# Kernel optimization log

Measured on AMD Instinct MI355X. Metric: run time of the kernel, lower is better.

The kernel has to match this reference:

```python
import jax, jax.numpy as jnp
import numpy as np
from jax import lax

B, T, D, H = 4, 4096, 1024, 8
DK, DV = 1024, 2048          # expand_k=1.0, expand_v=2.0
RANK, MAXL, LOOPD = 16, 8, 128  # lora_rank, max_loops, dim*loop_dim_fraction
THRESH = 0.99
EPS = 1e-6
GK_SCALE = 16.0              # GLA forget-gate temperature


def setup_inputs() -> dict:
    key = jax.random.key(0)
    ks = jax.random.split(key, 16)
    r = lambda i, shape, s=0.02: jax.random.normal(ks[i], shape, jnp.float32) * s
    return {
        "h": jax.random.normal(ks[0], (B, T, D), jnp.float32),
        "e": jax.random.normal(ks[1], (B, T, D), jnp.float32),
        "norm_w": jnp.ones((D,), jnp.float32),
        "out_norm_w": jnp.ones((D,), jnp.float32),
        "Wq": r(2, (D, DK)), "Wk": r(3, (D, DK)), "Wv": r(4, (D, DV)),
        "Wgk": r(5, (D, DK)), "Wg": r(6, (D, DV)), "Wo": r(7, (DV, D)),
        "lora_A": r(8, (MAXL, D, RANK)), "lora_B": r(9, (MAXL, RANK, D)),
        "inj_A": 0.9 * jnp.eye(D, dtype=jnp.float32) + r(10, (D, D)),
        "inj_B": r(11, (D, D)),
        "act_w": r(12, (D,)),
        "act_b": jnp.full((), -2.0, jnp.float32),  # gradual halting
        "loop_table": r(13, (MAXL, LOOPD)),
        "n_loops": 4,
    }


def rmsnorm(x, w):
    return x * lax.rsqrt(jnp.mean(x * x, axis=-1, keepdims=True) + EPS) * w


def gla(x, Wq, Wk, Wv, Wgk, Wg, Wo, num_heads):
    """Gated Linear Attention: data-dependent forget gates, linear-time recurrent scan."""
    b, t, d = x.shape
    dk, dv = Wq.shape[1], Wv.shape[1]
    dkh, dvh = dk // num_heads, dv // num_heads
    q = (x @ Wq).reshape(b, t, num_heads, dkh) * (dkh ** -0.5)
    k = (x @ Wk).reshape(b, t, num_heads, dkh)
    v = (x @ Wv).reshape(b, t, num_heads, dvh)
    # forget gate alpha in (0,1): exp(logsigmoid(gk)/16)
    alpha = jnp.exp(jax.nn.log_sigmoid(x @ Wgk) / GK_SCALE).reshape(b, t, num_heads, dkh)

    def step(S, qkva):  # S: (b, H, dkh, dvh)
        qt, kt, vt, at = qkva
        S = at[..., None] * S + kt[..., None] * vt[..., None, :]
        ot = jnp.einsum('bhk,bhkv->bhv', qt, S)
        return S, ot

    S0 = jnp.zeros((b, num_heads, dkh, dvh), x.dtype)
    xs = (jnp.swapaxes(q, 0, 1), jnp.swapaxes(k, 0, 1),
          jnp.swapaxes(v, 0, 1), jnp.swapaxes(alpha, 0, 1))
    _, o = lax.scan(step, S0, xs)                  # o: (t, b, H, dvh)
    o = jnp.swapaxes(o, 0, 1).reshape(b, t, dv)
    o = o * jax.nn.silu(x @ Wg)                    # output gate
    return o @ Wo


def reference(h, e, norm_w, out_norm_w, Wq, Wk, Wv, Wgk, Wg, Wo,
              lora_A, lora_B, inj_A, inj_B, act_w, act_b, loop_table, n_loops):
    b, t_len, d = h.shape
    halted = jnp.zeros((b, t_len), bool)
    cum = jnp.zeros((b, t_len), h.dtype)
    h_out = jnp.zeros_like(h)
    loopd = loop_table.shape[1]
    for t in range(n_loops):  # small fixed depth loop (structurally distinct LoRA/embed per t)
        # loop index embedding on first loopd channels
        h = h.at[..., :loopd].add(loop_table[t])
        h_norm = rmsnorm(h + e, norm_w)
        g = gla(h_norm, Wq, Wk, Wv, Wgk, Wg, Wo, H)   # dropout: eval mode (identity)
        g = g + (g @ lora_A[t]) @ lora_B[t]            # depth LoRA
        h = h @ inj_A.T + e @ inj_B.T + g              # LTI injection: A.h + B.e + gla
        # ACT halting accumulate
        p = jax.nn.sigmoid(h @ act_w + act_b)          # (b, t_len)
        running = ~halted
        p_eff = jnp.where(running, p, jnp.zeros_like(p))
        new_cum = cum + p_eff
        newly = running & (new_cum >= THRESH)
        w = jnp.where(newly, 1.0 - cum, p_eff)         # remainder for newly-halted
        h_out = h_out + w[..., None] * h
        cum = new_cum
        halted = halted | newly
    return rmsnorm(h_out, out_norm_w)
```

## Files before the change

kernel.cpp:

```cpp
#include <hip/hip_runtime.h>

#define BB 4
#define TT 4096
#define DD 1024
#define HH 8
#define DKK 1024
#define DVV 2048
#define MR (BB*TT)
#define DKH 128
#define DVH 256
#define NLOOPS 4
#define LCH 128
#define NCH (TT/LCH)
#define PADW 136
#define NPROJ 7168

#define WS_NEED 662310912ull

__device__ __attribute__((aligned(256))) unsigned char g_ws[WS_NEED];

typedef __bf16 bf16x8 __attribute__((ext_vector_type(8)));
typedef float  f32x4  __attribute__((ext_vector_type(4)));

__device__ __forceinline__ unsigned short f2bfu(float f) {
    unsigned int u = __builtin_bit_cast(unsigned int, f);
    u += 0x7fffu + ((u >> 16) & 1u);
    return (unsigned short)(u >> 16);
}
__device__ __forceinline__ float bfu2f(unsigned short s) {
    unsigned int u = ((unsigned int)s) << 16;
    return __builtin_bit_cast(float, u);
}

__device__ __forceinline__ void gld_lds16(const void* g, void* l) {
    __builtin_amdgcn_global_load_lds(
        (__attribute__((address_space(1))) void*)const_cast<void*>(g),
        (__attribute__((address_space(3))) void*)l, 16, 0, 0);
}

__global__ __launch_bounds__(256) void k_transpose_bf16(
    const float* __restrict__ in, unsigned short* __restrict__ out, int K, int N)
{
    __shared__ float tile[64][65];
    int k0 = blockIdx.y * 64, n0 = blockIdx.x * 64;
    int tx = threadIdx.x & 63, ty = threadIdx.x >> 6;
    #pragma unroll
    for (int r = 0; r < 64; r += 4)
        tile[ty + r][tx] = in[(size_t)(k0 + ty + r) * N + n0 + tx];
    __syncthreads();
    #pragma unroll
    for (int r = 0; r < 64; r += 4)
        out[(size_t)(n0 + ty + r) * K + k0 + tx] = f2bfu(tile[tx][ty + r]);
}

__global__ __launch_bounds__(256) void k_conv_e(
    const float* __restrict__ e, unsigned short* __restrict__ he)
{
    size_t gid = (size_t)blockIdx.x * 256 + threadIdx.x;
    size_t b4 = gid * 4;
    size_t row = b4 >> 10; int col = (int)(b4 & 1023);
    float4 v = *(const float4*)&e[row * 1024 + col];
    *(ushort4*)&he[row * 2048 + 1024 + col] =
        make_ushort4(f2bfu(v.x), f2bfu(v.y), f2bfu(v.z), f2bfu(v.w));
}

__global__ __launch_bounds__(256) void k_conv_injcomb(
    const float* __restrict__ injA, const float* __restrict__ injB,
    unsigned short* __restrict__ WinjT, float* __restrict__ diag)
{
    int idx = blockIdx.x * 256 + threadIdx.x;
    int i = idx >> 10, j = idx & 1023;
    float va = injA[idx], vb = injB[idx];
    unsigned short ua;
    if (i == j) { diag[i] = va; ua = 0; }
    else        { ua = f2bfu(va); }
    WinjT[(size_t)i * 2048 + j] = ua;
    WinjT[(size_t)i * 2048 + 1024 + j] = f2bfu(vb);
}

__global__ __launch_bounds__(256) void k_prep(
    float* __restrict__ h, const float* __restrict__ e,
    const float* __restrict__ norm_w, const float* __restrict__ ltab,
    unsigned short* __restrict__ he, unsigned short* __restrict__ xn_bf)
{
    int row = blockIdx.x, tid = threadIdx.x;
    size_t base = (size_t)row * DD + tid * 4;
    float4 hv = *(float4*)&h[base];
    if (tid < 32) {
        float4 lv = *(const float4*)&ltab[tid * 4];
        hv.x += lv.x; hv.y += lv.y; hv.z += lv.z; hv.w += lv.w;
        *(float4*)&h[base] = hv;
    }
    float4 ev = *(const float4*)&e[base];
    float sx = hv.x + ev.x, sy = hv.y + ev.y, sz = hv.z + ev.z, sw = hv.w + ev.w;
    float partial = sx*sx + sy*sy + sz*sz + sw*sw;
    __shared__ float red[256];
    red[tid] = partial; __syncthreads();
    for (int st = 128; st > 0; st >>= 1) {
        if (tid < st) red[tid] += red[tid + st];
        __syncthreads();
    }
    float rms = rsqrtf(red[0] * (1.0f / DD) + 1e-6f);
    float4 wv = *(const float4*)&norm_w[tid * 4];
    *(ushort4*)&xn_bf[base] = make_ushort4(
        f2bfu(sx * rms * wv.x), f2bfu(sy * rms * wv.y),
        f2bfu(sz * rms * wv.z), f2bfu(sw * rms * wv.w));
    *(ushort4*)&he[(size_t)row * 2048 + tid * 4] =
        make_ushort4(f2bfu(hv.x), f2bfu(hv.y), f2bfu(hv.z), f2bfu(hv.w));
}

template<int KB>
__device__ __forceinline__ void gemm8_core(
    const char* __restrict__ Ab, const char* __restrict__ Bb,
    int bm, int bn, char* sm, f32x4 (&acc)[8][4])
{
    constexpr int NKT = KB / 128;
    const int tid = threadIdx.x;
    const int lane = tid & 63;
    const int wave = tid >> 6;
    const int wm = wave >> 2, wn = wave & 3;
    const int ln15 = lane & 15, q4 = lane >> 4;
    const int xorv = (ln15 & 7) << 4;
    const int xc0 = (q4 * 16) ^ xorv;
    const int xc1 = (64 + q4 * 16) ^ xorv;

    const int L0 = tid * 16;
    const int L1 = 8192 + tid * 16;
    const int lin0 = L0 ^ (((L0 >> 7) & 7) << 4);
    const int lin1 = L1 ^ (((L1 >> 7) & 7) << 4);
    const int sr0 = lin0 >> 7, sc0 = lin0 & 127;
    const int sr1 = lin1 >> 7, sc1 = lin1 & 127;

    bf16x8 av[4][2];
    bf16x8 bv[2][2][2];

    auto STAGE = [&](const char* gb, int row0, int kcol, int region) {
        gld_lds16(gb + (size_t)(row0 + sr0) * KB + (kcol + sc0), sm + region + L0);
        gld_lds16(gb + (size_t)(row0 + sr1) * KB + (kcol + sc1), sm + region + L1);
    };

#define LD_AV(CB, MH) \
    _Pragma("unroll") \
    for (int i2 = 0; i2 < 4; ++i2) { \
        const char* rp = sm + (CB) + ((MH) * 16384) \
                       + ((wm * 64 + i2 * 16 + ln15) * 128); \
        av[i2][0] = *(const bf16x8*)(rp + xc0); \
        av[i2][1] = *(const bf16x8*)(rp + xc1); \
    }
#define LD_BV(CB, NH) \
    _Pragma("unroll") \
    for (int j2 = 0; j2 < 2; ++j2) { \
        const char* rp = sm + (CB) + 32768 + ((NH) * 16384) \
                       + ((wn * 32 + j2 * 16 + ln15) * 128); \
        bv[NH][j2][0] = *(const bf16x8*)(rp + xc0); \
        bv[NH][j2][1] = *(const bf16x8*)(rp + xc1); \
    }
#define MFMA_Q(MH, NH) \
    __builtin_amdgcn_s_setprio(1); \
    _Pragma("unroll") \
    for (int i2 = 0; i2 < 4; ++i2) \
        _Pragma("unroll") \
        for (int j2 = 0; j2 < 2; ++j2) { \
            acc[(MH)*4+i2][(NH)*2+j2] = __builtin_amdgcn_mfma_f32_16x16x32_bf16( \
                av[i2][0], bv[NH][j2][0], acc[(MH)*4+i2][(NH)*2+j2], 0, 0, 0); \
            acc[(MH)*4+i2][(NH)*2+j2] = __builtin_amdgcn_mfma_f32_16x16x32_bf16( \
                av[i2][1], bv[NH][j2][1], acc[(MH)*4+i2][(NH)*2+j2], 0, 0, 0); \
        } \
    __builtin_amdgcn_s_setprio(0);

    STAGE(Ab, bm,       0, 0);
    STAGE(Bb, bn,       0, 32768);
    STAGE(Bb, bn + 128, 0, 49152);
    STAGE(Ab, bm + 128, 0, 16384);

    #pragma unroll 2
    for (int kt = 0; kt < NKT - 1; ++kt) {
        const int cb = (kt & 1) << 16;
        const int sb = cb ^ 65536;
        const int kcol = (kt + 1) * 128;
        STAGE(Ab, bm, kcol, sb);
        asm volatile("s_waitcnt vmcnt(6)" ::: "memory");
        __builtin_amdgcn_s_barrier();
        LD_AV(cb, 0)
        LD_BV(cb, 0)
        MFMA_Q(0, 0)
        STAGE(Bb, bn, kcol, sb + 32768);
        asm volatile("s_waitcnt vmcnt(6)" ::: "memory");
        __builtin_amdgcn_s_barrier();
        LD_BV(cb, 1)
        MFMA_Q(0, 1)
        STAGE(Bb, bn + 128, kcol, sb + 49152);
        asm volatile("s_waitcnt vmcnt(6)" ::: "memory");
        __builtin_amdgcn_s_barrier();
        LD_AV(cb, 1)
        MFMA_Q(1, 1)
        STAGE(Ab, bm + 128, kcol, sb + 16384);
        MFMA_Q(1, 0)
    }
    {
        const int cb = ((NKT - 1) & 1) << 16;
        asm volatile("s_waitcnt vmcnt(4)" ::: "memory");
        __builtin_amdgcn_s_barrier();
        LD_AV(cb, 0)
        LD_BV(cb, 0)
        MFMA_Q(0, 0)
        asm volatile("s_waitcnt vmcnt(2)" ::: "memory");
        __builtin_amdgcn_s_barrier();
        LD_BV(cb, 1)
        MFMA_Q(0, 1)
        asm volatile("s_waitcnt vmcnt(0)" ::: "memory");
        __builtin_amdgcn_s_barrier();
        LD_AV(cb, 1)
        MFMA_Q(1, 1)
        MFMA_Q(1, 0)
    }
#undef LD_AV
#undef LD_BV
#undef MFMA_Q
}

__global__ __launch_bounds__(512, 2) void k_gemm_proj8(
    const unsigned short* __restrict__ A, const unsigned short* __restrict__ Bt,
    unsigned short* __restrict__ qout, unsigned short* __restrict__ kout,
    float* __restrict__ lgout, unsigned short* __restrict__ vout,
    unsigned short* __restrict__ xgout, float qscale)
{
    extern __shared__ char sm[];
    int bid = blockIdx.x;
    int nb = (bid & 7) * 224 + (bid >> 3);
    int bm = (nb / 28) * 256, bn = (nb % 28) * 256;

    f32x4 acc[8][4];
    #pragma unroll
    for (int i = 0; i < 8; ++i)
        #pragma unroll
        for (int j = 0; j < 4; ++j) { f32x4 z = {0,0,0,0}; acc[i][j] = z; }

    gemm8_core<2048>((const char*)A, (const char*)Bt, bm, bn, sm, acc);

    const int tid = threadIdx.x, lane = tid & 63, wave = tid >> 6;
    const int wm = wave >> 2, wn = wave & 3;
    const int ln15 = lane & 15, q4 = lane >> 4;

    if (bn >= 2048 && bn < 3072) {
        int cb = bn - 2048;
        #pragma unroll
        for (int fm = 0; fm < 8; ++fm) {
            int mh = fm >> 2, i2 = fm & 3;
            int rowb = bm + mh * 128 + wm * 64 + i2 * 16 + q4 * 4;
            #pragma unroll
            for (int fn = 0; fn < 4; ++fn) {
                int nh = fn >> 1, j2 = fn & 1;
                int col = cb + nh * 128 + wn * 32 + j2 * 16 + ln15;
                #pragma unroll
                for (int r = 0; r < 4; ++r) {
                    float v = acc[fm][fn][r];
                    v = (fminf(v, 0.f) - log1pf(expf(-fabsf(v)))) * 0.0625f;
                    lgout[(size_t)(rowb + r) * 1024 + col] = v;
                }
            }
        }
    } else {
        unsigned short* obuf; int stride, cb;
        float scale = 1.f;
        if (bn < 1024)      { obuf = qout;  stride = 1024; cb = bn;        scale = qscale; }
        else if (bn < 2048) { obuf = kout;  stride = 1024; cb = bn - 1024; }
        else if (bn < 5120) { obuf = vout;  stride = 2048; cb = bn - 3072; }
        else                { obuf = xgout; stride = 2048; cb = bn - 5120; }
        #pragma unroll
        for (int fm = 0; fm < 8; ++fm) {
            int mh = fm >> 2, i2 = fm & 3;
            int rowb = bm + mh * 128 + wm * 64 + i2 * 16 + q4 * 4;
            #pragma unroll
            for (int fn = 0; fn < 4; ++fn) {
                int nh = fn >> 1, j2 = fn & 1;
                int col = cb + nh * 128 + wn * 32 + j2 * 16 + ln15;
                #pragma unroll
                for (int r = 0; r < 4; ++r)
                    obuf[(size_t)(rowb + r) * stride + col] =
                        f2bfu(acc[fm][fn][r] * scale);
            }
        }
    }
}

template<int HASADD, int HASDIAG, int KB>
__global__ __launch_bounds__(512, 2) void k_gemm8_f32(
    const unsigned short* __restrict__ A, const unsigned short* __restrict__ Bt,
    float* __restrict__ out, const float* __restrict__ addend,
    const float* __restrict__ hsrc, const float* __restrict__ diag, int N)
{
    extern __shared__ char sm[];
    int bid = blockIdx.x;
    int cpx = gridDim.x >> 3;
    int nb = (bid & 7) * cpx + (bid >> 3);
    int nbn = N >> 8;
    int bm = (nb / nbn) * 256, bn = (nb % nbn) * 256;

    f32x4 acc[8][4];
    #pragma unroll
    for (int i = 0; i < 8; ++i)
        #pragma unroll
        for (int j = 0; j < 4; ++j) { f32x4 z = {0,0,0,0}; acc[i][j] = z; }

    gemm8_core<KB>((const char*)A, (const char*)Bt, bm, bn, sm, acc);

    const int tid = threadIdx.x, lane = tid & 63, wave = tid >> 6;
    const int wm = wave >> 2, wn = wave & 3;
    const int ln15 = lane & 15, q4 = lane >> 4;

    #pragma unroll
    for (int fm = 0; fm < 8; ++fm) {
        int mh = fm >> 2, i2 = fm & 3;
        int rowb = bm + mh * 128 + wm * 64 + i2 * 16 + q4 * 4;
        #pragma unroll
        for (int fn = 0; fn < 4; ++fn) {
            int nh = fn >> 1, j2 = fn & 1;
            int col = bn + nh * 128 + wn * 32 + j2 * 16 + ln15;
            float dg = 0.f;
            if (HASDIAG) dg = diag[col];
            #pragma unroll
            for (int r = 0; r < 4; ++r) {
                size_t oi = (size_t)(rowb + r) * N + col;
                float v = acc[fm][fn][r];
                if (HASDIAG) v += hsrc[oi] * dg;
                if (HASADD)  v += addend[oi];
                out[oi] = v;
            }
        }
    }
}

__global__ __launch_bounds__(256) void k_c1(
    const float* __restrict__ lg, unsigned short* __restrict__ q,
    unsigned short* __restrict__ kk, float* __restrict__ dLe)
{
    int chunk = blockIdx.x;
    int bh = blockIdx.y * 2 + (threadIdx.x >> 7);
    int b = bh >> 3, h = bh & 7;
    int i = threadIdx.x & 127;
    size_t r0 = (size_t)b * TT + (size_t)chunk * LCH;
    float c = 0.f, e = 1.f;
    for (int t = 0; t < LCH; ++t) {
        size_t off = (r0 + t) * DKK + h * DKH + i;
        c += lg[off];
        e = __expf(c);
        float ei = __expf(-c);
        q[off] = f2bfu(bfu2f(q[off]) * e);
        kk[off] = f2bfu(bfu2f(kk[off]) * ei);
    }
    dLe[((size_t)chunk * 32 + bh) * DKH + i] = e;
}

__global__ __launch_bounds__(256, 1) void k_c2(
    const unsigned short* __restrict__ q, const unsigned short* __restrict__ kk,
    const unsigned short* __restrict__ v, unsigned short* __restrict__ ob,
    float* __restrict__ U)
{
    extern __shared__ unsigned short smd[];
    unsigned short* lQ  = smd;
    unsigned short* lK  = smd + LCH * PADW;
    unsigned short* lKT = smd + 2 * LCH * PADW;
    unsigned short* lVT = smd + 3 * LCH * PADW;

    int chunk = blockIdx.x, bh = blockIdx.y;
    int b = bh >> 3, h = bh & 7;
    int tid = threadIdx.x, lane = tid & 63, wave = tid >> 6;
    int wm = wave >> 1, wn = wave & 1;
    int quad = lane >> 4, mr = lane & 15;
    size_t r0 = (size_t)b * TT + (size_t)chunk * LCH;

    #pragma unroll
    for (int ps = 0; ps < 8; ++ps) {
        int idx = ps * 256 + tid;
        int row = idx >> 4, c8 = (idx & 15) * 8;
        size_t g = (r0 + row) * DKK + h * DKH + c8;
        *(int4*)&lQ[row * PADW + c8] = *(const int4*)&q[g];
        union { int4 w; unsigned short u[8]; } tmp;
        tmp.w = *(const int4*)&kk[g];
        *(int4*)&lK[row * PADW + c8] = tmp.w;
        #pragma unroll
        for (int u2 = 0; u2 < 8; ++u2)
            lKT[(c8 + u2) * PADW + row] = tmp.u[u2];
    }
    __syncthreads();

    f32x4 pa[4][4];
    #pragma unroll
    for (int i = 0; i < 4; ++i)
        #pragma unroll
        for (int j = 0; j < 4; ++j) { f32x4 z = {0,0,0,0}; pa[i][j] = z; }
    for (int k0 = 0; k0 < DKH; k0 += 32) {
        bf16x8 av[4], bv[4];
        #pragma unroll
        for (int t2 = 0; t2 < 4; ++t2) {
            av[t2] = *(const bf16x8*)&lQ[(wm * 64 + t2 * 16 + mr) * PADW + k0 + quad * 8];
            bv[t2] = *(const bf16x8*)&lK[(wn * 64 + t2 * 16 + mr) * PADW + k0 + quad * 8];
        }
        #pragma unroll
        for (int tm = 0; tm < 4; ++tm)
            #pragma unroll
            for (int tn = 0; tn < 4; ++tn)
                pa[tm][tn] = __builtin_amdgcn_mfma_f32_16x16x32_bf16(
                    av[tm], bv[tn], pa[tm][tn], 0, 0, 0);
    }
    __syncthreads();

    #pragma unroll
    for (int tm = 0; tm < 4; ++tm)
        #pragma unroll
        for (int tn = 0; tn < 4; ++tn)
            #pragma unroll
            for (int r = 0; r < 4; ++r) {
                int trow = wm * 64 + tm * 16 + quad * 4 + r;
                int scol = wn * 64 + tn * 16 + mr;
                float pv = (trow >= scol) ? pa[tm][tn][r] : 0.f;
                lQ[trow * PADW + scol] = f2bfu(pv);
            }
    #pragma unroll
    for (int ps = 0; ps < 8; ++ps) {
        int idx = ps * 256 + tid;
        int s = idx >> 4, j8 = (idx & 15) * 8;
        size_t g = (r0 + s) * DVV + h * DVH + j8;
        union { int4 w; unsigned short u[8]; } tmp;
        tmp.w = *(const int4*)&v[g];
        #pragma unroll
        for (int u2 = 0; u2 < 8; ++u2)
            lVT[(j8 + u2) * PADW + s] = tmp.u[u2];
    }
    __syncthreads();

    #pragma unroll 1
    for (int panel = 0; panel < 2; ++panel) {
        f32x4 oa[4][4], ua[4][4];
        #pragma unroll
        for (int i = 0; i < 4; ++i)
            #pragma unroll
            for (int j = 0; j < 4; ++j) { f32x4 z = {0,0,0,0}; oa[i][j] = z; ua[i][j] = z; }
        for (int k0 = 0; k0 < LCH; k0 += 32) {
            bf16x8 pv[4], kt[4], vb[4];
            #pragma unroll
            for (int t2 = 0; t2 < 4; ++t2) {
                pv[t2] = *(const bf16x8*)&lQ [(wm * 64 + t2 * 16 + mr) * PADW + k0 + quad * 8];
                kt[t2] = *(const bf16x8*)&lKT[(wm * 64 + t2 * 16 + mr) * PADW + k0 + quad * 8];
                vb[t2] = *(const bf16x8*)&lVT[(wn * 64 + t2 * 16 + mr) * PADW + k0 + quad * 8];
            }
            #pragma unroll
            for (int tm = 0; tm < 4; ++tm)
                #pragma unroll
                for (int tn = 0; tn < 4; ++tn) {
                    oa[tm][tn] = __builtin_amdgcn_mfma_f32_16x16x32_bf16(
                        pv[tm], vb[tn], oa[tm][tn], 0, 0, 0);
                    ua[tm][tn] = __builtin_amdgcn_mfma_f32_16x16x32_bf16(
                        kt[tm], vb[tn], ua[tm][tn], 0, 0, 0);
                }
        }
        #pragma unroll
        for (int tm = 0; tm < 4; ++tm)
            #pragma unroll
            for (int tn = 0; tn < 4; ++tn)
                #pragma unroll
                for (int r = 0; r < 4; ++r) {
                    int m_ = wm * 64 + tm * 16 + quad * 4 + r;
                    int j_ = panel * 128 + wn * 64 + tn * 16 + mr;
                    ob[(r0 + m_) * DVV + h * DVH + j_] = f2bfu(oa[tm][tn][r]);
                    U[(((size_t)chunk * 32 + bh) * DKH + m_) * DVH + j_] = ua[tm][tn][r];
                }
        __syncthreads();
        if (panel == 0) {
            #pragma unroll
            for (int ps = 0; ps < 8; ++ps) {
                int idx = ps * 256 + tid;
                int s = idx >> 4, j8 = (idx & 15) * 8;
                size_t g = (r0 + s) * DVV + h * DVH + 128 + j8;
                union { int4 w; unsigned short u[8]; } tmp;
                tmp.w = *(const int4*)&v[g];
                #pragma unroll
                for (int u2 = 0; u2 < 8; ++u2)
                    lVT[(j8 + u2) * PADW + s] = tmp.u[u2];
            }
            __syncthreads();
        }
    }
}

__global__ __launch_bounds__(256) void k_c3(
    float* __restrict__ U, const float* __restrict__ dLe)
{
    int gid = blockIdx.x * 256 + threadIdx.x;
    int bh = gid >> 13;
    int rem = gid & 8191;
    int i = rem >> 6, j4 = rem & 63;
    float4 S = make_float4(0.f, 0.f, 0.f, 0.f);
    for (int c = 0; c < NCH; ++c) {
        size_t off = (((size_t)c * 32 + bh) * DKH + i) * DVH + j4 * 4;
        float4 u = *(float4*)&U[off];
        *(float4*)&U[off] = S;
        float d = dLe[((size_t)c * 32 + bh) * DKH + i];
        S.x = d * (S.x + u.x); S.y = d * (S.y + u.y);
        S.z = d * (S.z + u.z); S.w = d * (S.w + u.w);
    }
}

__global__ __launch_bounds__(256, 1) void k_c4(
    const unsigned short* __restrict__ q, const float* __restrict__ S,
    unsigned short* __restrict__ ob, const unsigned short* __restrict__ xg)
{
    extern __shared__ unsigned short smd[];
    unsigned short* lQ  = smd;
    unsigned short* lST = smd + LCH * PADW;

    int chunk = blockIdx.x, bh = blockIdx.y;
    int b = bh >> 3, h = bh & 7;
    int tid = threadIdx.x, lane = tid & 63, wave = tid >> 6;
    int wm = wave >> 1, wn = wave & 1;
    int quad = lane >> 4, mr = lane & 15;
    size_t r0 = (size_t)b * TT + (size_t)chunk * LCH;

    #pragma unroll
    for (int ps = 0; ps < 8; ++ps) {
        int idx = ps * 256 + tid;
        int row = idx >> 4, c8 = (idx & 15) * 8;
        size_t g = (r0 + row) * DKK + h * DKH + c8;
        *(int4*)&lQ[row * PADW + c8] = *(const int4*)&q[g];
    }

    #pragma unroll 1
    for (int panel = 0; panel < 2; ++panel) {
        __syncthreads();
        #pragma unroll
        for (int ps = 0; ps < 16; ++ps) {
            int idx = ps * 256 + tid;
            int i = idx >> 5, j4 = idx & 31;
            float4 sv = *(const float4*)&S[(((size_t)chunk * 32 + bh) * DKH + i) * DVH
                                           + panel * 128 + j4 * 4];
            lST[(j4 * 4 + 0) * PADW + i] = f2bfu(sv.x);
            lST[(j4 * 4 + 1) * PADW + i] = f2bfu(sv.y);
            lST[(j4 * 4 + 2) * PADW + i] = f2bfu(sv.z);
            lST[(j4 * 4 + 3) * PADW + i] = f2bfu(sv.w);
        }
        __syncthreads();

        f32x4 oa[4][4];
        #pragma unroll
        for (int i = 0; i < 4; ++i)
            #pragma unroll
            for (int j = 0; j < 4; ++j) { f32x4 z = {0,0,0,0}; oa[i][j] = z; }
        for (int k0 = 0; k0 < DKH; k0 += 32) {
            bf16x8 av[4], bv[4];
            #pragma unroll
            for (int t2 = 0; t2 < 4; ++t2) {
                av[t2] = *(const bf16x8*)&lQ [(wm * 64 + t2 * 16 + mr) * PADW + k0 + quad * 8];
                bv[t2] = *(const bf16x8*)&lST[(wn * 64 + t2 * 16 + mr) * PADW + k0 + quad * 8];
            }
            #pragma unroll
            for (int tm = 0; tm < 4; ++tm)
                #pragma unroll
                for (int tn = 0; tn < 4; ++tn)
                    oa[tm][tn] = __builtin_amdgcn_mfma_f32_16x16x32_bf16(
                        av[tm], bv[tn], oa[tm][tn], 0, 0, 0);
        }
        #pragma unroll
        for (int tm = 0; tm < 4; ++tm)
            #pragma unroll
            for (int tn = 0; tn < 4; ++tn)
                #pragma unroll
                for (int r = 0; r < 4; ++r) {
                    int t_ = wm * 64 + tm * 16 + quad * 4 + r;
                    int j_ = panel * 128 + wn * 64 + tn * 16 + mr;
                    size_t oi = (r0 + t_) * DVV + h * DVH + j_;
                    float ov = bfu2f(ob[oi]) + oa[tm][tn][r];
                    float xf = bfu2f(xg[oi]);
                    ob[oi] = f2bfu(ov * xf / (1.f + expf(-xf)));
                }
    }
}

__global__ __launch_bounds__(256) void k_lora1(
    const float* __restrict__ G, const float* __restrict__ A, float* __restrict__ tmp)
{
    int row = blockIdx.x * 4 + (threadIdx.x >> 6);
    int lane = threadIdx.x & 63;
    float acc[16];
    #pragma unroll
    for (int r = 0; r < 16; ++r) acc[r] = 0.f;
    const float* grow = G + (size_t)row * DD;
    for (int k2 = lane; k2 < DD; k2 += 64) {
        float g = grow[k2];
        const float4* ar = (const float4*)(A + k2 * 16);
        float4 a0 = ar[0], a1 = ar[1], a2 = ar[2], a3 = ar[3];
        acc[0] = fmaf(g, a0.x, acc[0]);  acc[1] = fmaf(g, a0.y, acc[1]);
        acc[2] = fmaf(g, a0.z, acc[2]);  acc[3] = fmaf(g, a0.w, acc[3]);
        acc[4] = fmaf(g, a1.x, acc[4]);  acc[5] = fmaf(g, a1.y, acc[5]);
        acc[6] = fmaf(g, a1.z, acc[6]);  acc[7] = fmaf(g, a1.w, acc[7]);
        acc[8] = fmaf(g, a2.x, acc[8]);  acc[9] = fmaf(g, a2.y, acc[9]);
        acc[10] = fmaf(g, a2.z, acc[10]); acc[11] = fmaf(g, a2.w, acc[11]);
        acc[12] = fmaf(g, a3.x, acc[12]); acc[13] = fmaf(g, a3.y, acc[13]);
        acc[14] = fmaf(g, a3.z, acc[14]); acc[15] = fmaf(g, a3.w, acc[15]);
    }
    #pragma unroll
    for (int off = 32; off >= 1; off >>= 1)
        #pragma unroll
        for (int r = 0; r < 16; ++r) acc[r] += __shfl_xor(acc[r], off);
    if (lane == 0) {
        #pragma unroll
        for (int r = 0; r < 16; ++r) tmp[(size_t)row * 16 + r] = acc[r];
    }
}

__global__ __launch_bounds__(256) void k_lora2(
    float* __restrict__ G, const float* __restrict__ tmp, const float* __restrict__ Bm)
{
    int row = blockIdx.x, tid = threadIdx.x;
    __shared__ float t16[16];
    if (tid < 16) t16[tid] = tmp[(size_t)row * 16 + tid];
    __syncthreads();
    size_t base = (size_t)row * DD + tid * 4;
    float4 acc = *(float4*)&G[base];
    #pragma unroll
    for (int r = 0; r < 16; ++r) {
        float tv = t16[r];
        float4 bv = *(const float4*)&Bm[r * DD + tid * 4];
        acc.x = fmaf(tv, bv.x, acc.x); acc.y = fmaf(tv, bv.y, acc.y);
        acc.z = fmaf(tv, bv.z, acc.z); acc.w = fmaf(tv, bv.w, acc.w);
    }
    *(float4*)&G[base] = acc;
}

__global__ __launch_bounds__(256) void k_act(
    const float* __restrict__ h, const float* __restrict__ act_w,
    const float* __restrict__ act_b, float* __restrict__ out,
    float* __restrict__ cum, int* __restrict__ halted)
{
    int row = blockIdx.x, tid = threadIdx.x;
    size_t base = (size_t)row * DD + tid * 4;
    float4 hv = *(const float4*)&h[base];
    float4 wv = *(const float4*)&act_w[tid * 4];
    float partial = hv.x*wv.x + hv.y*wv.y + hv.z*wv.z + hv.w*wv.w;
    __shared__ float red[256];
    __shared__ float s_cm;
    __shared__ int s_hl;
    if (tid == 0) { s_cm = cum[row]; s_hl = halted[row]; }
    red[tid] = partial; __syncthreads();
    for (int st = 128; st > 0; st >>= 1) {
        if (tid < st) red[tid] += red[tid + st];
        __syncthreads();
    }
    float p = 1.f / (1.f + expf(-(red[0] + act_b[0])));
    float cm = s_cm;
    int hl = s_hl;
    float p_eff = hl ? 0.f : p;
    float ncum = cm + p_eff;
    int newly = (!hl) && (ncum >= 0.99f);
    float w = newly ? (1.f - cm) : p_eff;
    float4 ho = *(float4*)&out[base];
    ho.x += w * hv.x; ho.y += w * hv.y; ho.z += w * hv.z; ho.w += w * hv.w;
    *(float4*)&out[base] = ho;
    if (tid == 0) { cum[row] = ncum; halted[row] = hl | newly; }
}

__global__ __launch_bounds__(256) void k_final(
    float* __restrict__ io, const float* __restrict__ w)
{
    int row = blockIdx.x, tid = threadIdx.x;
    size_t base = (size_t)row * DD + tid * 4;
    float4 hv = *(const float4*)&io[base];
    float partial = hv.x*hv.x + hv.y*hv.y + hv.z*hv.z + hv.w*hv.w;
    __shared__ float red[256];
    red[tid] = partial; __syncthreads();
    for (int st = 128; st > 0; st >>= 1) {
        if (tid < st) red[tid] += red[tid + st];
        __syncthreads();
    }
    float rms = rsqrtf(red[0] * (1.0f / DD) + 1e-6f);
    float4 wv = *(const float4*)&w[tid * 4];
    float4 o = make_float4(hv.x*rms*wv.x, hv.y*rms*wv.y, hv.z*rms*wv.z, hv.w*rms*wv.w);
    *(float4*)&io[base] = o;
}

extern "C" void kernel_launch(void* const* d_in, const int* in_sizes, int n_in,
                              void* d_out, int out_size, void* d_ws, size_t ws_size,
                              hipStream_t stream)
{
    const float* in_h       = (const float*)d_in[0];
    const float* in_e       = (const float*)d_in[1];
    const float* norm_w     = (const float*)d_in[2];
    const float* out_norm_w = (const float*)d_in[3];
    const float* Wq   = (const float*)d_in[4];
    const float* Wk   = (const float*)d_in[5];
    const float* Wv   = (const float*)d_in[6];
    const float* Wgk  = (const float*)d_in[7];
    const float* Wg   = (const float*)d_in[8];
    const float* Wo   = (const float*)d_in[9];
    const float* lora_A = (const float*)d_in[10];
    const float* lora_B = (const float*)d_in[11];
    const float* inj_A  = (const float*)d_in[12];
    const float* inj_B  = (const float*)d_in[13];
    const float* act_w  = (const float*)d_in[14];
    const float* act_b  = (const float*)d_in[15];
    const float* loop_table = (const float*)d_in[16];

    char* p;
    if (ws_size >= WS_NEED) {
        p = (char*)d_ws;
    } else {
        void* sym = nullptr;
        hipGetSymbolAddress(&sym, HIP_SYMBOL(g_ws));
        p = (char*)sym;
    }

    float* h      = (float*)p;            p += (size_t)MR * DD * 4;
    unsigned short* he_bf = (unsigned short*)p; p += (size_t)MR * 2048 * 2;
    unsigned short* xn_bf = (unsigned short*)p; p += (size_t)MR * DD * 2;
    unsigned short* q_bf  = (unsigned short*)p; p += (size_t)MR * DKK * 2;
    unsigned short* k_bf  = (unsigned short*)p; p += (size_t)MR * DKK * 2;
    unsigned short* v_bf  = (unsigned short*)p; p += (size_t)MR * DVV * 2;
    unsigned short* xg_bf = (unsigned short*)p; p += (size_t)MR * DVV * 2;
    float* lgbuf  = (float*)p;            p += (size_t)MR * DKK * 4;
    unsigned short* ob0   = (unsigned short*)p; p += (size_t)MR * DVV * 2;
    float* U      = (float*)p;            p += (size_t)NCH * 32 * DKH * DVH * 4;
    float* dLe    = (float*)p;            p += (size_t)NCH * 32 * DKH * 4;
    unsigned short* WprojT = (unsigned short*)p; p += (size_t)NPROJ * DKK * 2;
    unsigned short* WoT    = (unsigned short*)p; p += (size_t)DD * DVV * 2;
    unsigned short* WinjT  = (unsigned short*)p; p += (size_t)DD * 2048 * 2;
    float* diagA = (float*)p;             p += DD * 4;
    float* tmp16 = (float*)p;             p += (size_t)MR * 16 * 4;
    float* cum   = (float*)p;             p += MR * 4;
    int*   halted = (int*)p;              p += MR * 4;
    float* g2 = lgbuf;
    float* h_out = (float*)d_out;

    hipMemcpyAsync(h, in_h, (size_t)MR * DD * 4, hipMemcpyDeviceToDevice, stream);
    hipMemsetAsync(h_out, 0, (size_t)MR * DD * 4, stream);
    hipMemsetAsync(cum, 0, MR * 4, stream);
    hipMemsetAsync(halted, 0, MR * 4, stream);

    k_transpose_bf16<<<dim3(16, 16), 256, 0, stream>>>(Wq,  WprojT,              DD, DKK);
    k_transpose_bf16<<<dim3(16, 16), 256, 0, stream>>>(Wk,  WprojT + 1024*1024,  DD, DKK);
    k_transpose_bf16<<<dim3(16, 16), 256, 0, stream>>>(Wgk, WprojT + 2048*1024,  DD, DKK);
    k_transpose_bf16<<<dim3(32, 16), 256, 0, stream>>>(Wv,  WprojT + 3072*1024,  DD, DVV);
    k_transpose_bf16<<<dim3(32, 16), 256, 0, stream>>>(Wg,  WprojT + (size_t)5120*1024, DD, DVV);
    k_transpose_bf16<<<dim3(16, 32), 256, 0, stream>>>(Wo,  WoT, DVV, DD);
    k_conv_injcomb<<<4096, 256, 0, stream>>>(inj_A, inj_B, WinjT, diagA);
    k_conv_e<<<MR * DD / 1024, 256, 0, stream>>>(in_e, he_bf);

    const float qscale = 0.08838834764831845f;

    for (int t = 0; t < NLOOPS; ++t) {
        k_prep<<<MR, 256, 0, stream>>>(h, in_e, norm_w, loop_table + t * 128, he_bf, xn_bf);

        k_gemm_proj8<<<1792, 512, 131072, stream>>>(
            xn_bf, WprojT, q_bf, k_bf, lgbuf, v_bf, xg_bf, qscale);

        k_c1<<<dim3(NCH, 16), 256, 0, stream>>>(lgbuf, q_bf, k_bf, dLe);
        k_c2<<<dim3(NCH, 32), 256, 4 * LCH * PADW * 2, stream>>>(
            q_bf, k_bf, v_bf, ob0, U);
        k_c3<<<1024, 256, 0, stream>>>(U, dLe);
        k_c4<<<dim3(NCH, 32), 256, 2 * LCH * PADW * 2, stream>>>(q_bf, U, ob0, xg_bf);

        k_gemm8_f32<0, 0, 4096><<<256, 512, 131072, stream>>>(
            ob0, WoT, g2, nullptr, nullptr, nullptr, DD);

        k_lora1<<<MR / 4, 256, 0, stream>>>(g2, lora_A + (size_t)t * DD * 16, tmp16);
        k_lora2<<<MR, 256, 0, stream>>>(g2, tmp16, lora_B + (size_t)t * 16 * DD);

        k_gemm8_f32<1, 1, 4096><<<256, 512, 131072, stream>>>(
            he_bf, WinjT, h, g2, h, diagA, DD);

        k_act<<<MR, 256, 0, stream>>>(h, act_w, act_b, h_out, cum, halted);
    }

    k_final<<<MR, 256, 0, stream>>>(h_out, out_norm_w);
}
```

Measured before the change: 4.177 ms.

## Interleave GEMM epilogue with final MFMA quadrants and widen chunk kernel to 8 waves

The shared GEMM core now takes an epilogue callback that stores each accumulator quadrant as soon as its last MFMAs finish. This lets global stores overlap with the remaining matrix math instead of running after it. The first-quadrant B load is hoisted, which removes one barrier/waitcnt per k-step, and the wait counts are retuned to match. The intra-chunk kernel k_c2 moves from 4 to 8 waves per block, with each wave covering half the columns, to raise parallelism. The risks are more register pressure, and a stale-LDS hazard if the new wait counts do not cover the hoisted B loads.

```diff
diff --git a/kernel.cpp b/kernel.cpp
--- a/kernel.cpp
+++ b/kernel.cpp
@@ -22,6 +22,8 @@
 typedef __bf16 bf16x8 __attribute__((ext_vector_type(8)));
 typedef float  f32x4  __attribute__((ext_vector_type(4)));
 
+template<int N> struct IC { static constexpr int v = N; };
+
 __device__ __forceinline__ unsigned short f2bfu(float f) {
     unsigned int u = __builtin_bit_cast(unsigned int, f);
     u += 0x7fffu + ((u >> 16) & 1u);
@@ -108,36 +110,6 @@
     *(ushort4*)&he[(size_t)row * 2048 + tid * 4] =
         make_ushort4(f2bfu(hv.x), f2bfu(hv.y), f2bfu(hv.z), f2bfu(hv.w));
 }
-
-template<int KB>
-__device__ __forceinline__ void gemm8_core(
-    const char* __restrict__ Ab, const char* __restrict__ Bb,
-    int bm, int bn, char* sm, f32x4 (&acc)[8][4])
-{
-    constexpr int NKT = KB / 128;
-    const int tid = threadIdx.x;
-    const int lane = tid & 63;
-    const int wave = tid >> 6;
-    const int wm = wave >> 2, wn = wave & 3;
-    const int ln15 = lane & 15, q4 = lane >> 4;
-    const int xorv = (ln15 & 7) << 4;
-    const int xc0 = (q4 * 16) ^ xorv;
-    const int xc1 = (64 + q4 * 16) ^ xorv;
-
-    const int L0 = tid * 16;
-    const int L1 = 8192 + tid * 16;
-    const int lin0 = L0 ^ (((L0 >> 7) & 7) << 4);
-    const int lin1 = L1 ^ (((L1 >> 7) & 7) << 4);
-    const int sr0 = lin0 >> 7, sc0 = lin0 & 127;
-    const int sr1 = lin1 >> 7, sc1 = lin1 & 127;
-
-    bf16x8 av[4][2];
-    bf16x8 bv[2][2][2];
-
-    auto STAGE = [&](const char* gb, int row0, int kcol, int region) {
-        gld_lds16(gb + (size_t)(row0 + sr0) * KB + (kcol + sc0), sm + region + L0);
-        gld_lds16(gb + (size_t)(row0 + sr1) * KB + (kcol + sc1), sm + region + L1);
-    };
 
 #define LD_AV(CB, MH) \
     _Pragma("unroll") \
@@ -168,6 +140,37 @@
         } \
     __builtin_amdgcn_s_setprio(0);
 
+template<int KB, class EPI>
+__device__ __forceinline__ void gemm8_core(
+    const char* __restrict__ Ab, const char* __restrict__ Bb,
+    int bm, int bn, char* sm, f32x4 (&acc)[8][4], EPI&& epi)
+{
+    constexpr int NKT = KB / 128;
+    const int tid = threadIdx.x;
+    const int lane = tid & 63;
+    const int wave = tid >> 6;
+    const int wm = wave >> 2, wn = wave & 3;
+    const int ln15 = lane & 15, q4 = lane >> 4;
+    (void)q4;
+    const int xorv = (ln15 & 7) << 4;
+    const int xc0 = (q4 * 16) ^ xorv;
+    const int xc1 = (64 + q4 * 16) ^ xorv;
+
+    const int L0 = tid * 16;
+    const int L1 = 8192 + tid * 16;
+    const int lin0 = L0 ^ (((L0 >> 7) & 7) << 4);
+    const int lin1 = L1 ^ (((L1 >> 7) & 7) << 4);
+    const int sr0 = lin0 >> 7, sc0 = lin0 & 127;
+    const int sr1 = lin1 >> 7, sc1 = lin1 & 127;
+
+    bf16x8 av[4][2];
+    bf16x8 bv[2][2][2];
+
+    auto STAGE = [&](const char* gb, int row0, int kcol, int region) {
+        gld_lds16(gb + (size_t)(row0 + sr0) * KB + (kcol + sc0), sm + region + L0);
+        gld_lds16(gb + (size_t)(row0 + sr1) * KB + (kcol + sc1), sm + region + L1);
+    };
+
     STAGE(Ab, bm,       0, 0);
     STAGE(Bb, bn,       0, 32768);
     STAGE(Bb, bn + 128, 0, 49152);
@@ -179,15 +182,13 @@
         const int sb = cb ^ 65536;
         const int kcol = (kt + 1) * 128;
         STAGE(Ab, bm, kcol, sb);
-        asm volatile("s_waitcnt vmcnt(6)" ::: "memory");
+        asm volatile("s_waitcnt vmcnt(4)" ::: "memory");
         __builtin_amdgcn_s_barrier();
         LD_AV(cb, 0)
         LD_BV(cb, 0)
+        LD_BV(cb, 1)
         MFMA_Q(0, 0)
         STAGE(Bb, bn, kcol, sb + 32768);
-        asm volatile("s_waitcnt vmcnt(6)" ::: "memory");
-        __builtin_amdgcn_s_barrier();
-        LD_BV(cb, 1)
         MFMA_Q(0, 1)
         STAGE(Bb, bn + 128, kcol, sb + 49152);
         asm volatile("s_waitcnt vmcnt(6)" ::: "memory");
@@ -199,24 +200,23 @@
     }
     {
         const int cb = ((NKT - 1) & 1) << 16;
-        asm volatile("s_waitcnt vmcnt(4)" ::: "memory");
+        asm volatile("s_waitcnt vmcnt(2)" ::: "memory");
         __builtin_amdgcn_s_barrier();
         LD_AV(cb, 0)
         LD_BV(cb, 0)
+        LD_BV(cb, 1)
         MFMA_Q(0, 0)
-        asm volatile("s_waitcnt vmcnt(2)" ::: "memory");
-        __builtin_amdgcn_s_barrier();
-        LD_BV(cb, 1)
+        epi(IC<0>{}, IC<0>{});
         MFMA_Q(0, 1)
+        epi(IC<0>{}, IC<1>{});
         asm volatile("s_waitcnt vmcnt(0)" ::: "memory");
         __builtin_amdgcn_s_barrier();
         LD_AV(cb, 1)
         MFMA_Q(1, 1)
+        epi(IC<1>{}, IC<1>{});
         MFMA_Q(1, 0)
-    }
-#undef LD_AV
-#undef LD_BV
-#undef MFMA_Q
+        epi(IC<1>{}, IC<0>{});
+    }
 }
 
 __global__ __launch_bounds__(512, 2) void k_gemm_proj8(
@@ -230,58 +230,60 @@
     int nb = (bid & 7) * 224 + (bid >> 3);
     int bm = (nb / 28) * 256, bn = (nb % 28) * 256;
 
-    f32x4 acc[8][4];
-    #pragma unroll
-    for (int i = 0; i < 8; ++i)
-        #pragma unroll
-        for (int j = 0; j < 4; ++j) { f32x4 z = {0,0,0,0}; acc[i][j] = z; }
-
-    gemm8_core<2048>((const char*)A, (const char*)Bt, bm, bn, sm, acc);
-
     const int tid = threadIdx.x, lane = tid & 63, wave = tid >> 6;
     const int wm = wave >> 2, wn = wave & 3;
     const int ln15 = lane & 15, q4 = lane >> 4;
 
-    if (bn >= 2048 && bn < 3072) {
-        int cb = bn - 2048;
-        #pragma unroll
-        for (int fm = 0; fm < 8; ++fm) {
-            int mh = fm >> 2, i2 = fm & 3;
-            int rowb = bm + mh * 128 + wm * 64 + i2 * 16 + q4 * 4;
-            #pragma unroll
-            for (int fn = 0; fn < 4; ++fn) {
-                int nh = fn >> 1, j2 = fn & 1;
-                int col = cb + nh * 128 + wn * 32 + j2 * 16 + ln15;
+    const bool islg = (bn >= 2048 && bn < 3072);
+    const int lgc = bn - 2048;
+    unsigned short* obuf = qout; int stride = 1024, cbc = bn;
+    float scale = 1.f;
+    if (bn < 1024)          { scale = qscale; }
+    else if (bn < 2048)     { obuf = kout;  cbc = bn - 1024; }
+    else if (bn >= 5120)    { obuf = xgout; stride = 2048; cbc = bn - 5120; }
+    else if (bn >= 3072)    { obuf = vout;  stride = 2048; cbc = bn - 3072; }
+
+    f32x4 acc[8][4];
+    #pragma unroll
+    for (int i = 0; i < 8; ++i)
+        #pragma unroll
+        for (int j = 0; j < 4; ++j) { f32x4 z = {0,0,0,0}; acc[i][j] = z; }
+
+    auto epi = [&](auto MHt, auto NHt) {
+        constexpr int mh = decltype(MHt)::v;
+        constexpr int nh = decltype(NHt)::v;
+        if (islg) {
+            #pragma unroll
+            for (int i2 = 0; i2 < 4; ++i2) {
+                int rowb = bm + mh * 128 + wm * 64 + i2 * 16 + q4 * 4;
                 #pragma unroll
-                for (int r = 0; r < 4; ++r) {
-                    float v = acc[fm][fn][r];
-                    v = (fminf(v, 0.f) - log1pf(expf(-fabsf(v)))) * 0.0625f;
-                    lgout[(size_t)(rowb + r) * 1024 + col] = v;
+                for (int j2 = 0; j2 < 2; ++j2) {
+                    int col = lgc + nh * 128 + wn * 32 + j2 * 16 + ln15;
+                    #pragma unroll
+                    for (int r = 0; r < 4; ++r) {
+                        float v = acc[mh * 4 + i2][nh * 2 + j2][r];
+                        v = (fminf(v, 0.f) - log1pf(expf(-fabsf(v)))) * 0.0625f;
+                        lgout[(size_t)(rowb + r) * 1024 + col] = v;
+                    }
+                }
+            }
+        } else {
+            #pragma unroll
+            for (int i2 = 0; i2 < 4; ++i2) {
+                int rowb = bm + mh * 128 + wm * 64 + i2 * 16 + q4 * 4;
+                #pragma unroll
+                for (int j2 = 0; j2 < 2; ++j2) {
+                    int col = cbc + nh * 128 + wn * 32 + j2 * 16 + ln15;
+                    #pragma unroll
+                    for (int r = 0; r < 4; ++r)
+                        obuf[(size_t)(rowb + r) * stride + col] =
+                            f2bfu(acc[mh * 4 + i2][nh * 2 + j2][r] * scale);
                 }
             }
         }
-    } else {
-        unsigned short* obuf; int stride, cb;
-        float scale = 1.f;
-        if (bn < 1024)      { obuf = qout;  stride = 1024; cb = bn;        scale = qscale; }
-        else if (bn < 2048) { obuf = kout;  stride = 1024; cb = bn - 1024; }
-        else if (bn < 5120) { obuf = vout;  stride = 2048; cb = bn - 3072; }
-        else                { obuf = xgout; stride = 2048; cb = bn - 5120; }
-        #pragma unroll
-        for (int fm = 0; fm < 8; ++fm) {
-            int mh = fm >> 2, i2 = fm & 3;
-            int rowb = bm + mh * 128 + wm * 64 + i2 * 16 + q4 * 4;
-            #pragma unroll
-            for (int fn = 0; fn < 4; ++fn) {
-                int nh = fn >> 1, j2 = fn & 1;
-                int col = cb + nh * 128 + wn * 32 + j2 * 16 + ln15;
-                #pragma unroll
-                for (int r = 0; r < 4; ++r)
-                    obuf[(size_t)(rowb + r) * stride + col] =
-                        f2bfu(acc[fm][fn][r] * scale);
-            }
-        }
-    }
+    };
+
+    gemm8_core<2048>((const char*)A, (const char*)Bt, bm, bn, sm, acc, epi);
 }
 
 template<int HASADD, int HASDIAG, int KB>
@@ -297,39 +299,45 @@
     int nbn = N >> 8;
     int bm = (nb / nbn) * 256, bn = (nb % nbn) * 256;
 
-    f32x4 acc[8][4];
-    #pragma unroll
-    for (int i = 0; i < 8; ++i)
-        #pragma unroll
-        for (int j = 0; j < 4; ++j) { f32x4 z = {0,0,0,0}; acc[i][j] = z; }
-
-    gemm8_core<KB>((const char*)A, (const char*)Bt, bm, bn, sm, acc);
-
     const int tid = threadIdx.x, lane = tid & 63, wave = tid >> 6;
     const int wm = wave >> 2, wn = wave & 3;
     const int ln15 = lane & 15, q4 = lane >> 4;
 
-    #pragma unroll
-    for (int fm = 0; fm < 8; ++fm) {
-        int mh = fm >> 2, i2 = fm & 3;
-        int rowb = bm + mh * 128 + wm * 64 + i2 * 16 + q4 * 4;
-        #pragma unroll
-        for (int fn = 0; fn < 4; ++fn) {
-            int nh = fn >> 1, j2 = fn & 1;
-            int col = bn + nh * 128 + wn * 32 + j2 * 16 + ln15;
-            float dg = 0.f;
-            if (HASDIAG) dg = diag[col];
-            #pragma unroll
-            for (int r = 0; r < 4; ++r) {
-                size_t oi = (size_t)(rowb + r) * N + col;
-                float v = acc[fm][fn][r];
-                if (HASDIAG) v += hsrc[oi] * dg;
-                if (HASADD)  v += addend[oi];
-                out[oi] = v;
+    f32x4 acc[8][4];
+    #pragma unroll
+    for (int i = 0; i < 8; ++i)
+        #pragma unroll
+        for (int j = 0; j < 4; ++j) { f32x4 z = {0,0,0,0}; acc[i][j] = z; }
+
+    auto epi = [&](auto MHt, auto NHt) {
+        constexpr int mh = decltype(MHt)::v;
+        constexpr int nh = decltype(NHt)::v;
+        #pragma unroll
+        for (int i2 = 0; i2 < 4; ++i2) {
+            int rowb = bm + mh * 128 + wm * 64 + i2 * 16 + q4 * 4;
+            #pragma unroll
+            for (int j2 = 0; j2 < 2; ++j2) {
+                int col = bn + nh * 128 + wn * 32 + j2 * 16 + ln15;
+                float dg = 0.f;
+                if (HASDIAG) dg = diag[col];
+                #pragma unroll
+                for (int r = 0; r < 4; ++r) {
+                    size_t oi = (size_t)(rowb + r) * N + col;
+                    float v = acc[mh * 4 + i2][nh * 2 + j2][r];
+                    if (HASDIAG) v += hsrc[oi] * dg;
+                    if (HASADD)  v += addend[oi];
+                    out[oi] = v;
+                }
             }
         }
-    }
-}
+    };
+
+    gemm8_core<KB>((const char*)A, (const char*)Bt, bm, bn, sm, acc, epi);
+}
+
+#undef LD_AV
+#undef LD_BV
+#undef MFMA_Q
 
 __global__ __launch_bounds__(256) void k_c1(
     const float* __restrict__ lg, unsigned short* __restrict__ q,
@@ -352,7 +360,7 @@
     dLe[((size_t)chunk * 32 + bh) * DKH + i] = e;
 }
 
-__global__ __launch_bounds__(256, 1) void k_c2(
+__global__ __launch_bounds__(512, 1) void k_c2(
     const unsigned short* __restrict__ q, const unsigned short* __restrict__ kk,
     const unsigned short* __restrict__ v, unsigned short* __restrict__ ob,
     float* __restrict__ U)
@@ -366,13 +374,13 @@
     int chunk = blockIdx.x, bh = blockIdx.y;
     int b = bh >> 3, h = bh & 7;
     int tid = threadIdx.x, lane = tid & 63, wave = tid >> 6;
-    int wm = wave >> 1, wn = wave & 1;
+    int wm = wave >> 2, wn = wave & 3;
     int quad = lane >> 4, mr = lane & 15;
     size_t r0 = (size_t)b * TT + (size_t)chunk * LCH;
 
     #pragma unroll
-    for (int ps = 0; ps < 8; ++ps) {
-        int idx = ps * 256 + tid;
+    for (int ps = 0; ps < 4; ++ps) {
+        int idx = ps * 512 + tid;
         int row = idx >> 4, c8 = (idx & 15) * 8;
         size_t g = (r0 + row) * DKK + h * DKH + c8;
         *(int4*)&lQ[row * PADW + c8] = *(const int4*)&q[g];
@@ -385,41 +393,42 @@
     }
     __syncthreads();
 
-    f32x4 pa[4][4];
+    f32x4 pa[4][2];
     #pragma unroll
     for (int i = 0; i < 4; ++i)
         #pragma unroll
-        for (int j = 0; j < 4; ++j) { f32x4 z = {0,0,0,0}; pa[i][j] = z; }
+        for (int j = 0; j < 2; ++j) { f32x4 z = {0,0,0,0}; pa[i][j] = z; }
     for (int k0 = 0; k0 < DKH; k0 += 32) {
-        bf16x8 av[4], bv[4];
-        #pragma unroll
-        for (int t2 = 0; t2 < 4; ++t2) {
+        bf16x8 av[4], bvv[2];
+        #pragma unroll
+        for (int t2 = 0; t2 < 4; ++t2)
             av[t2] = *(const bf16x8*)&lQ[(wm * 64 + t2 * 16 + mr) * PADW + k0 + quad * 8];
-            bv[t2] = *(const bf16x8*)&lK[(wn * 64 + t2 * 16 + mr) * PADW + k0 + quad * 8];
-        }
+        #pragma unroll
+        for (int tn = 0; tn < 2; ++tn)
+            bvv[tn] = *(const bf16x8*)&lK[(wn * 32 + tn * 16 + mr) * PADW + k0 + quad * 8];
         #pragma unroll
         for (int tm = 0; tm < 4; ++tm)
             #pragma unroll
-            for (int tn = 0; tn < 4; ++tn)
+            for (int tn = 0; tn < 2; ++tn)
                 pa[tm][tn] = __builtin_amdgcn_mfma_f32_16x16x32_bf16(
-                    av[tm], bv[tn], pa[tm][tn], 0, 0, 0);
+                    av[tm], bvv[tn], pa[tm][tn], 0, 0, 0);
     }
     __syncthreads();
 
     #pragma unroll
     for (int tm = 0; tm < 4; ++tm)
         #pragma unroll
-        for (int tn = 0; tn < 4; ++tn)
+        for (int tn = 0; tn < 2; ++tn)
             #pragma unroll
             for (int r = 0; r < 4; ++r) {
                 int trow = wm * 64 + tm * 16 + quad * 4 + r;
-                int scol = wn * 64 + tn * 16 + mr;
+                int scol = wn * 32 + tn * 16 + mr;
                 float pv = (trow >= scol) ? pa[tm][tn][r] : 0.f;
                 lQ[trow * PADW + scol] = f2bfu(pv);
             }
     #pragma unroll
-    for (int ps = 0; ps < 8; ++ps) {
-        int idx = ps * 256 + tid;
+    for (int ps = 0; ps < 4; ++ps) {
+        int idx = ps * 512 + tid;
         int s = idx >> 4, j8 = (idx & 15) * 8;
         size_t g = (r0 + s) * DVV + h * DVH + j8;
         union { int4 w; unsigned short u[8]; } tmp;
@@ -432,23 +441,25 @@
 
     #pragma unroll 1
     for (int panel = 0; panel < 2; ++panel) {
-        f32x4 oa[4][4], ua[4][4];
+        f32x4 oa[4][2], ua[4][2];
         #pragma unroll
         for (int i = 0; i < 4; ++i)
             #pragma unroll
-            for (int j = 0; j < 4; ++j) { f32x4 z = {0,0,0,0}; oa[i][j] = z; ua[i][j] = z; }
+            for (int j = 0; j < 2; ++j) { f32x4 z = {0,0,0,0}; oa[i][j] = z; ua[i][j] = z; }
         for (int k0 = 0; k0 < LCH; k0 += 32) {
-            bf16x8 pv[4], kt[4], vb[4];
+            bf16x8 pv[4], kt[4], vb[2];
             #pragma unroll
             for (int t2 = 0; t2 < 4; ++t2) {
                 pv[t2] = *(const bf16x8*)&lQ [(wm * 64 + t2 * 16 + mr) * PADW + k0 + quad * 8];
                 kt[t2] = *(const bf16x8*)&lKT[(wm * 64 + t2 * 16 + mr) * PADW + k0 + quad * 8];
-                vb[t2] = *(const bf16x8*)&lVT[(wn * 64 + t2 * 16 + mr) * PADW + k0 + quad * 8];
             }
+            #pragma unroll
+            for (int tn = 0; tn < 2; ++tn)
+                vb[tn] = *(const bf16x8*)&lVT[(wn * 32 + tn * 16 + mr) * PADW + k0 + quad * 8];
             #pragma unroll
             for (int tm = 0; tm < 4; ++tm)
                 #pragma unroll
-                for (int tn = 0; tn < 4; ++tn) {
+                for (int tn = 0; tn < 2; ++tn) {
                     oa[tm][tn] = __builtin_amdgcn_mfma_f32_16x16x32_bf16(
                         pv[tm], vb[tn], oa[tm][tn], 0, 0, 0);
                     ua[tm][tn] = __builtin_amdgcn_mfma_f32_16x16x32_bf16(
@@ -458,19 +469,19 @@
         #pragma unroll
         for (int tm = 0; tm < 4; ++tm)
             #pragma unroll
-            for (int tn = 0; tn < 4; ++tn)
+            for (int tn = 0; tn < 2; ++tn)
                 #pragma unroll
                 for (int r = 0; r < 4; ++r) {
                     int m_ = wm * 64 + tm * 16 + quad * 4 + r;
-                    int j_ = panel * 128 + wn * 64 + tn * 16 + mr;
+                    int j_ = panel * 128 + wn * 32 + tn * 16 + mr;
                     ob[(r0 + m_) * DVV + h * DVH + j_] = f2bfu(oa[tm][tn][r]);
                     U[(((size_t)chunk * 32 + bh) * DKH + m_) * DVH + j_] = ua[tm][tn][r];
                 }
         __syncthreads();
         if (panel == 0) {
             #pragma unroll
-            for (int ps = 0; ps < 8; ++ps) {
-                int idx = ps * 256 + tid;
+            for (int ps = 0; ps < 4; ++ps) {
+                int idx = ps * 512 + tid;
                 int s = idx >> 4, j8 = (idx & 15) * 8;
                 size_t g = (r0 + s) * DVV + h * DVH + 128 + j8;
                 union { int4 w; unsigned short u[8]; } tmp;
@@ -547,18 +558,18 @@
             #pragma unroll
             for (int j = 0; j < 4; ++j) { f32x4 z = {0,0,0,0}; oa[i][j] = z; }
         for (int k0 = 0; k0 < DKH; k0 += 32) {
-            bf16x8 av[4], bv[4];
+            bf16x8 av[4], bvv[4];
             #pragma unroll
             for (int t2 = 0; t2 < 4; ++t2) {
                 av[t2] = *(const bf16x8*)&lQ [(wm * 64 + t2 * 16 + mr) * PADW + k0 + quad * 8];
-                bv[t2] = *(const bf16x8*)&lST[(wn * 64 + t2 * 16 + mr) * PADW + k0 + quad * 8];
+                bvv[t2] = *(const bf16x8*)&lST[(wn * 64 + t2 * 16 + mr) * PADW + k0 + quad * 8];
             }
             #pragma unroll
             for (int tm = 0; tm < 4; ++tm)
                 #pragma unroll
                 for (int tn = 0; tn < 4; ++tn)
                     oa[tm][tn] = __builtin_amdgcn_mfma_f32_16x16x32_bf16(
-                        av[tm], bv[tn], oa[tm][tn], 0, 0, 0);
+                        av[tm], bvv[tn], oa[tm][tn], 0, 0, 0);
         }
         #pragma unroll
         for (int tm = 0; tm < 4; ++tm)
@@ -753,7 +764,7 @@
             xn_bf, WprojT, q_bf, k_bf, lgbuf, v_bf, xg_bf, qscale);
 
         k_c1<<<dim3(NCH, 16), 256, 0, stream>>>(lgbuf, q_bf, k_bf, dLe);
-        k_c2<<<dim3(NCH, 32), 256, 4 * LCH * PADW * 2, stream>>>(
+        k_c2<<<dim3(NCH, 32), 512, 4 * LCH * PADW * 2, stream>>>(
             q_bf, k_bf, v_bf, ob0, U);
         k_c3<<<1024, 256, 0, stream>>>(U, dLe);
         k_c4<<<dim3(NCH, 32), 256, 2 * LCH * PADW * 2, stream>>>(q_bf, U, ob0, xg_bf);
```

Result: slower. 4.377 ms (+4.8%).
